# Kernel optimization log

Hardware: AMD Instinct MI355X
Metric: run time of the kernel (lower is better)

## Reference

```python
import jax, jax.numpy as jnp
import numpy as np

N_NODES = 1_000_000
N_UPD = 131_072
H = 128        # memory_dim
D_MSG = 256    # message_dim


def setup_inputs() -> dict:
    key = jax.random.key(0)
    ks = jax.random.split(key, 7)
    s_ih = 1.0 / np.sqrt(H)
    return {
        "memory": jax.random.normal(ks[0], (N_NODES, H), dtype=jnp.float32),
        "node_ids": jax.random.randint(ks[1], (N_UPD,), 0, N_NODES),
        "messages": jax.random.normal(ks[2], (N_UPD, D_MSG), dtype=jnp.float32),
        "W_ih": jax.random.uniform(ks[3], (3 * H, D_MSG), minval=-s_ih, maxval=s_ih, dtype=jnp.float32),
        "W_hh": jax.random.uniform(ks[4], (3 * H, H), minval=-s_ih, maxval=s_ih, dtype=jnp.float32),
        "b_ih": jax.random.uniform(ks[5], (3 * H,), minval=-s_ih, maxval=s_ih, dtype=jnp.float32),
        "b_hh": jax.random.uniform(ks[6], (3 * H,), minval=-s_ih, maxval=s_ih, dtype=jnp.float32),
    }


def _gru_cell(x, h, W_ih, W_hh, b_ih, b_hh):
    # torch GRUCell math. gates laid out as [r, z, n] along dim 0 of weights.
    gi = x @ W_ih.T + b_ih            # [M, 3H]
    gh = h @ W_hh.T + b_hh            # [M, 3H]
    i_r, i_z, i_n = jnp.split(gi, 3, axis=-1)
    h_r, h_z, h_n = jnp.split(gh, 3, axis=-1)
    r = jax.nn.sigmoid(i_r + h_r)
    z = jax.nn.sigmoid(i_z + h_z)
    n = jnp.tanh(i_n + r * h_n)
    return (1.0 - z) * n + z * h


def reference(memory, node_ids, messages, W_ih, W_hh, b_ih, b_hh):
    node_mem = memory[node_ids]                              # gather [M, H]
    updated = _gru_cell(messages, node_mem, W_ih, W_hh, b_ih, b_hh)
    return memory.at[node_ids].set(updated)                  # scatter back into full table
```

## Files before the change

### kernel.cpp

```cpp
#include <hip/hip_runtime.h>
#include <math.h>

#define NN     1000000
#define NUPD   131072
#define HDIM   128
#define DMSG   256
#define GRU_BLOCKS (NUPD / 64)
#define COPY_BLOCKS 4096

#define WI_OFF  0
#define WH_OFF  (384 * 256 * 2)
#define WIN_OFF (WH_OFF + 384 * 128 * 2)

typedef __attribute__((ext_vector_type(8))) short bf16x8;
typedef __attribute__((ext_vector_type(4))) float f32x4;

__device__ __forceinline__ short f2bf(float f) {
  unsigned u = __float_as_uint(f);
  unsigned r = (u + 0x7fffu + ((u >> 16) & 1u)) >> 16;
  return (short)r;
}
__device__ __forceinline__ float sigmoidf_fast(float x) {
  return 1.0f / (1.0f + __expf(-x));
}
__device__ __forceinline__ float tanhf_fast(float x) {
  return 1.0f - 2.0f / (__expf(2.0f * x) + 1.0f);
}

__global__ void mark_winner_kernel(const int* __restrict__ ids,
                                   int* __restrict__ w) {
  int j = blockIdx.x * blockDim.x + threadIdx.x;
  if (j < NUPD) atomicMax(&w[ids[j]], j);
}

__global__ void wconv_kernel(const float* __restrict__ Wi,
                             const float* __restrict__ Wh,
                             short* __restrict__ wi_bf,
                             short* __restrict__ wh_bf) {
  int i = blockIdx.x * blockDim.x + threadIdx.x;
  if (i < 384 * 256) {
    wi_bf[i] = f2bf(Wi[i]);
  } else {
    int j = i - 384 * 256;
    if (j < 384 * 128) wh_bf[j] = f2bf(Wh[j]);
  }
}

__launch_bounds__(512, 2)
__global__ void fat_kernel(const float* __restrict__ memory,
                           const int* __restrict__ node_ids,
                           const float* __restrict__ messages,
                           const short* __restrict__ Wi_bf,
                           const short* __restrict__ Wh_bf,
                           const float* __restrict__ b_ih,
                           const float* __restrict__ b_hh,
                           const int* __restrict__ winner,
                           float* __restrict__ out)
{
  __shared__ short xs[64][DMSG + 8];
  __shared__ short hs[64][HDIM + 8];
  __shared__ int   ids_s[64];
  __shared__ char  flag_s[64];

  const int tid = threadIdx.x;

  if (blockIdx.x >= GRU_BLOCKS) {
    const float4* __restrict__ src4 = (const float4*)memory;
    float4* __restrict__ dst4 = (float4*)out;
    const long long n4 = (long long)NN * (HDIM / 4);
    long long i = (long long)(blockIdx.x - GRU_BLOCKS) * 512 + tid;
    const long long stride = (long long)COPY_BLOCKS * 512;
    for (; i < n4; i += stride) {
      int row = (int)(i >> 5);
      if (winner[row] < 0) dst4[i] = src4[i];
    }
    return;
  }

  const int row0 = blockIdx.x * 64;
  const int lane = tid & 63;
  const int wv   = tid >> 6;

  if (tid < 64) {
    int id = node_ids[row0 + tid];
    ids_s[tid] = id;
    flag_s[tid] = (winner[id] == row0 + tid) ? 1 : 0;
  }

  {
    int r = tid >> 5;
    int c8 = tid & 31;
#pragma unroll
    for (int it = 0; it < 4; ++it) {
      const float4* p4 = (const float4*)(messages + (size_t)(row0 + r + it * 16) * DMSG);
      float4 v0 = p4[c8 * 2];
      float4 v1 = p4[c8 * 2 + 1];
      bf16x8 o;
      o[0] = f2bf(v0.x); o[1] = f2bf(v0.y); o[2] = f2bf(v0.z); o[3] = f2bf(v0.w);
      o[4] = f2bf(v1.x); o[5] = f2bf(v1.y); o[6] = f2bf(v1.z); o[7] = f2bf(v1.w);
      *(bf16x8*)&xs[r + it * 16][c8 * 8] = o;
    }
  }

  {
    int r = tid >> 3;
    int c16 = (tid & 7) * 16;
    int id = node_ids[row0 + r];
    const float4* p4 = (const float4*)(memory + (size_t)id * HDIM + c16);
    float4 v0 = p4[0], v1 = p4[1], v2 = p4[2], v3 = p4[3];
    bf16x8 o0, o1;
    o0[0] = f2bf(v0.x); o0[1] = f2bf(v0.y); o0[2] = f2bf(v0.z); o0[3] = f2bf(v0.w);
    o0[4] = f2bf(v1.x); o0[5] = f2bf(v1.y); o0[6] = f2bf(v1.z); o0[7] = f2bf(v1.w);
    o1[0] = f2bf(v2.x); o1[1] = f2bf(v2.y); o1[2] = f2bf(v2.z); o1[3] = f2bf(v2.w);
    o1[4] = f2bf(v3.x); o1[5] = f2bf(v3.y); o1[6] = f2bf(v3.z); o1[7] = f2bf(v3.w);
    *(bf16x8*)&hs[r][c16] = o0;
    *(bf16x8*)&hs[r][c16 + 8] = o1;
  }

  __syncthreads();

  const int g0  = __builtin_amdgcn_readfirstlane(wv * 16);
  const int col = lane & 15;
  const int kg  = lane >> 4;

  f32x4 acc_r[4]  = {{0,0,0,0},{0,0,0,0},{0,0,0,0},{0,0,0,0}};
  f32x4 acc_z[4]  = {{0,0,0,0},{0,0,0,0},{0,0,0,0},{0,0,0,0}};
  f32x4 acc_in[4] = {{0,0,0,0},{0,0,0,0},{0,0,0,0},{0,0,0,0}};
  f32x4 acc_hn[4] = {{0,0,0,0},{0,0,0,0},{0,0,0,0},{0,0,0,0}};

  {
    const short* wr = Wi_bf + (size_t)(g0 + col) * DMSG;
    const short* wz = Wi_bf + (size_t)(g0 + 128 + col) * DMSG;
    const short* wn = Wi_bf + (size_t)(g0 + 256 + col) * DMSG;
#pragma unroll
    for (int ks = 0; ks < 8; ++ks) {
      const int ko = ks * 32 + kg * 8;
      bf16x8 br = *(const bf16x8*)(wr + ko);
      bf16x8 bz = *(const bf16x8*)(wz + ko);
      bf16x8 bn = *(const bf16x8*)(wn + ko);
#pragma unroll
      for (int rt = 0; rt < 4; ++rt) {
        bf16x8 a = *(const bf16x8*)&xs[rt * 16 + col][ko];
        acc_r[rt]  = __builtin_amdgcn_mfma_f32_16x16x32_bf16(a, br, acc_r[rt], 0, 0, 0);
        acc_z[rt]  = __builtin_amdgcn_mfma_f32_16x16x32_bf16(a, bz, acc_z[rt], 0, 0, 0);
        acc_in[rt] = __builtin_amdgcn_mfma_f32_16x16x32_bf16(a, bn, acc_in[rt], 0, 0, 0);
      }
    }
  }

  {
    const short* wr = Wh_bf + (size_t)(g0 + col) * HDIM;
    const short* wz = Wh_bf + (size_t)(g0 + 128 + col) * HDIM;
    const short* wn = Wh_bf + (size_t)(g0 + 256 + col) * HDIM;
#pragma unroll
    for (int ks = 0; ks < 4; ++ks) {
      const int ko = ks * 32 + kg * 8;
      bf16x8 br = *(const bf16x8*)(wr + ko);
      bf16x8 bz = *(const bf16x8*)(wz + ko);
      bf16x8 bn = *(const bf16x8*)(wn + ko);
#pragma unroll
      for (int rt = 0; rt < 4; ++rt) {
        bf16x8 a = *(const bf16x8*)&hs[rt * 16 + col][ko];
        acc_r[rt]  = __builtin_amdgcn_mfma_f32_16x16x32_bf16(a, br, acc_r[rt], 0, 0, 0);
        acc_z[rt]  = __builtin_amdgcn_mfma_f32_16x16x32_bf16(a, bz, acc_z[rt], 0, 0, 0);
        acc_hn[rt] = __builtin_amdgcn_mfma_f32_16x16x32_bf16(a, bn, acc_hn[rt], 0, 0, 0);
      }
    }
  }

  const int g = g0 + col;
  const float bias_r  = b_ih[g] + b_hh[g];
  const float bias_z  = b_ih[g + 128] + b_hh[g + 128];
  const float bias_in = b_ih[g + 256];
  const float bias_hn = b_hh[g + 256];

#pragma unroll
  for (int rt = 0; rt < 4; ++rt) {
#pragma unroll
    for (int reg = 0; reg < 4; ++reg) {
      const int row = rt * 16 + kg * 4 + reg;
      const int id  = ids_s[row];
      float r = sigmoidf_fast(acc_r[rt][reg] + bias_r);
      float z = sigmoidf_fast(acc_z[rt][reg] + bias_z);
      float n = tanhf_fast(acc_in[rt][reg] + bias_in + r * (acc_hn[rt][reg] + bias_hn));
      float h = memory[(size_t)id * HDIM + g];
      float nh = (1.0f - z) * n + z * h;
      if (flag_s[row]) out[(size_t)id * HDIM + g] = nh;
    }
  }
}

extern "C" void kernel_launch(void* const* d_in, const int* in_sizes, int n_in,
                              void* d_out, int out_size, void* d_ws, size_t ws_size,
                              hipStream_t stream) {
  const float* memory   = (const float*)d_in[0];
  const int*   node_ids = (const int*)  d_in[1];
  const float* messages = (const float*)d_in[2];
  const float* W_ih     = (const float*)d_in[3];
  const float* W_hh     = (const float*)d_in[4];
  const float* b_ih     = (const float*)d_in[5];
  const float* b_hh     = (const float*)d_in[6];
  float* out = (float*)d_out;

  char* ws = (char*)d_ws;
  short* Wi_bf  = (short*)(ws + WI_OFF);
  short* Wh_bf  = (short*)(ws + WH_OFF);
  int*   winner = (int*)  (ws + WIN_OFF);

  hipMemsetAsync(winner, 0xFF, (size_t)NN * sizeof(int), stream);
  mark_winner_kernel<<<NUPD / 256, 256, 0, stream>>>(node_ids, winner);
  wconv_kernel<<<(384 * 256 + 384 * 128 + 255) / 256, 256, 0, stream>>>(
      W_ih, W_hh, Wi_bf, Wh_bf);

  fat_kernel<<<GRU_BLOCKS + COPY_BLOCKS, 512, 0, stream>>>(
      memory, node_ids, messages, Wi_bf, Wh_bf, b_ih, b_hh, winner, out);
}
```

Measured before the change: 355.5 us.

## Interleave copy and GRU blocks, shrink GRU tiles, batch winner loads, merge prep kernels

```diff
diff --git a/kernel.cpp b/kernel.cpp
--- a/kernel.cpp
+++ b/kernel.cpp
@@ -5,8 +5,14 @@
 #define NUPD   131072
 #define HDIM   128
 #define DMSG   256
-#define GRU_BLOCKS (NUPD / 64)
-#define COPY_BLOCKS 4096
+
+#define GRU_ROWS    16
+#define GRU_BLOCKS  (NUPD / GRU_ROWS)
+#define COPY_BLOCKS 8192
+#define TOTAL_BLOCKS (GRU_BLOCKS + COPY_BLOCKS)
+#define COPY_STRIDE  (COPY_BLOCKS * 256)
+#define COPY_ITERS   16
+#define N4_TOTAL     ((long long)NN * (HDIM / 4))
 
 #define WI_OFF  0
 #define WH_OFF  (384 * 256 * 2)
@@ -27,26 +33,20 @@
   return 1.0f - 2.0f / (__expf(2.0f * x) + 1.0f);
 }
 
-__global__ void mark_winner_kernel(const int* __restrict__ ids,
-                                   int* __restrict__ w) {
-  int j = blockIdx.x * blockDim.x + threadIdx.x;
-  if (j < NUPD) atomicMax(&w[ids[j]], j);
-}
-
-__global__ void wconv_kernel(const float* __restrict__ Wi,
-                             const float* __restrict__ Wh,
-                             short* __restrict__ wi_bf,
-                             short* __restrict__ wh_bf) {
-  int i = blockIdx.x * blockDim.x + threadIdx.x;
-  if (i < 384 * 256) {
-    wi_bf[i] = f2bf(Wi[i]);
-  } else {
-    int j = i - 384 * 256;
-    if (j < 384 * 128) wh_bf[j] = f2bf(Wh[j]);
-  }
-}
-
-__launch_bounds__(512, 2)
+__global__ void prep_kernel(const int* __restrict__ ids,
+                            const float* __restrict__ Wi,
+                            const float* __restrict__ Wh,
+                            short* __restrict__ wi_bf,
+                            short* __restrict__ wh_bf,
+                            int* __restrict__ winner) {
+  int i = blockIdx.x * 256 + threadIdx.x;
+  if (i < NUPD) atomicMax(&winner[ids[i]], i);
+  if (i < 384 * 256) wi_bf[i] = f2bf(Wi[i]);
+  int j = i - 384 * 256;
+  if (j >= 0 && j < 384 * 128) wh_bf[j] = f2bf(Wh[j]);
+}
+
+__launch_bounds__(256, 5)
 __global__ void fat_kernel(const float* __restrict__ memory,
                            const int* __restrict__ node_ids,
                            const float* __restrict__ messages,
@@ -57,132 +57,127 @@
                            const int* __restrict__ winner,
                            float* __restrict__ out)
 {
-  __shared__ short xs[64][DMSG + 8];
-  __shared__ short hs[64][HDIM + 8];
-  __shared__ int   ids_s[64];
-  __shared__ char  flag_s[64];
+  __shared__ short xs[GRU_ROWS][DMSG + 8];
+  __shared__ short hs[GRU_ROWS][HDIM + 8];
+  __shared__ int   ids_s[GRU_ROWS];
+  __shared__ char  flag_s[GRU_ROWS];
 
   const int tid = threadIdx.x;
 
-  if (blockIdx.x >= GRU_BLOCKS) {
+  if (blockIdx.x & 1) {
+    const int ci = blockIdx.x >> 1;
     const float4* __restrict__ src4 = (const float4*)memory;
     float4* __restrict__ dst4 = (float4*)out;
-    const long long n4 = (long long)NN * (HDIM / 4);
-    long long i = (long long)(blockIdx.x - GRU_BLOCKS) * 512 + tid;
-    const long long stride = (long long)COPY_BLOCKS * 512;
-    for (; i < n4; i += stride) {
-      int row = (int)(i >> 5);
-      if (winner[row] < 0) dst4[i] = src4[i];
+    const long long base = (long long)ci * 256 + tid;
+
+    int w[COPY_ITERS];
+#pragma unroll
+    for (int it = 0; it < COPY_ITERS; ++it) {
+      long long i = base + (long long)it * COPY_STRIDE;
+      w[it] = (i < N4_TOTAL) ? winner[(int)(i >> 5)] : 0;
+    }
+#pragma unroll
+    for (int it = 0; it < COPY_ITERS; ++it) {
+      long long i = base + (long long)it * COPY_STRIDE;
+      if (i < N4_TOTAL && w[it] < 0) dst4[i] = src4[i];
     }
     return;
   }
 
-  const int row0 = blockIdx.x * 64;
+  const int gi   = blockIdx.x >> 1;
+  const int row0 = gi * GRU_ROWS;
   const int lane = tid & 63;
   const int wv   = tid >> 6;
 
-  if (tid < 64) {
+  if (tid < GRU_ROWS) {
     int id = node_ids[row0 + tid];
     ids_s[tid] = id;
     flag_s[tid] = (winner[id] == row0 + tid) ? 1 : 0;
   }
 
   {
-    int r = tid >> 5;
-    int c8 = tid & 31;
-#pragma unroll
-    for (int it = 0; it < 4; ++it) {
-      const float4* p4 = (const float4*)(messages + (size_t)(row0 + r + it * 16) * DMSG);
-      float4 v0 = p4[c8 * 2];
-      float4 v1 = p4[c8 * 2 + 1];
-      bf16x8 o;
-      o[0] = f2bf(v0.x); o[1] = f2bf(v0.y); o[2] = f2bf(v0.z); o[3] = f2bf(v0.w);
-      o[4] = f2bf(v1.x); o[5] = f2bf(v1.y); o[6] = f2bf(v1.z); o[7] = f2bf(v1.w);
-      *(bf16x8*)&xs[r + it * 16][c8 * 8] = o;
-    }
-  }
-
-  {
-    int r = tid >> 3;
-    int c16 = (tid & 7) * 16;
-    int id = node_ids[row0 + r];
-    const float4* p4 = (const float4*)(memory + (size_t)id * HDIM + c16);
+    int r = tid >> 4;
+    int c16 = (tid & 15) * 16;
+    const float4* p4 = (const float4*)(messages + (size_t)(row0 + r) * DMSG + c16);
     float4 v0 = p4[0], v1 = p4[1], v2 = p4[2], v3 = p4[3];
     bf16x8 o0, o1;
     o0[0] = f2bf(v0.x); o0[1] = f2bf(v0.y); o0[2] = f2bf(v0.z); o0[3] = f2bf(v0.w);
     o0[4] = f2bf(v1.x); o0[5] = f2bf(v1.y); o0[6] = f2bf(v1.z); o0[7] = f2bf(v1.w);
     o1[0] = f2bf(v2.x); o1[1] = f2bf(v2.y); o1[2] = f2bf(v2.z); o1[3] = f2bf(v2.w);
     o1[4] = f2bf(v3.x); o1[5] = f2bf(v3.y); o1[6] = f2bf(v3.z); o1[7] = f2bf(v3.w);
-    *(bf16x8*)&hs[r][c16] = o0;
-    *(bf16x8*)&hs[r][c16 + 8] = o1;
+    *(bf16x8*)&xs[r][c16]     = o0;
+    *(bf16x8*)&xs[r][c16 + 8] = o1;
+  }
+
+  {
+    int r = tid >> 4;
+    int c8 = (tid & 15) * 8;
+    int id = node_ids[row0 + r];
+    const float4* p4 = (const float4*)(memory + (size_t)id * HDIM + c8);
+    float4 v0 = p4[0], v1 = p4[1];
+    bf16x8 o;
+    o[0] = f2bf(v0.x); o[1] = f2bf(v0.y); o[2] = f2bf(v0.z); o[3] = f2bf(v0.w);
+    o[4] = f2bf(v1.x); o[5] = f2bf(v1.y); o[6] = f2bf(v1.z); o[7] = f2bf(v1.w);
+    *(bf16x8*)&hs[r][c8] = o;
   }
 
   __syncthreads();
 
-  const int g0  = __builtin_amdgcn_readfirstlane(wv * 16);
+  const int c0  = __builtin_amdgcn_readfirstlane(wv * 32);
   const int col = lane & 15;
   const int kg  = lane >> 4;
 
-  f32x4 acc_r[4]  = {{0,0,0,0},{0,0,0,0},{0,0,0,0},{0,0,0,0}};
-  f32x4 acc_z[4]  = {{0,0,0,0},{0,0,0,0},{0,0,0,0},{0,0,0,0}};
-  f32x4 acc_in[4] = {{0,0,0,0},{0,0,0,0},{0,0,0,0},{0,0,0,0}};
-  f32x4 acc_hn[4] = {{0,0,0,0},{0,0,0,0},{0,0,0,0},{0,0,0,0}};
-
-  {
-    const short* wr = Wi_bf + (size_t)(g0 + col) * DMSG;
-    const short* wz = Wi_bf + (size_t)(g0 + 128 + col) * DMSG;
-    const short* wn = Wi_bf + (size_t)(g0 + 256 + col) * DMSG;
-#pragma unroll
-    for (int ks = 0; ks < 8; ++ks) {
-      const int ko = ks * 32 + kg * 8;
-      bf16x8 br = *(const bf16x8*)(wr + ko);
-      bf16x8 bz = *(const bf16x8*)(wz + ko);
-      bf16x8 bn = *(const bf16x8*)(wn + ko);
-#pragma unroll
-      for (int rt = 0; rt < 4; ++rt) {
-        bf16x8 a = *(const bf16x8*)&xs[rt * 16 + col][ko];
-        acc_r[rt]  = __builtin_amdgcn_mfma_f32_16x16x32_bf16(a, br, acc_r[rt], 0, 0, 0);
-        acc_z[rt]  = __builtin_amdgcn_mfma_f32_16x16x32_bf16(a, bz, acc_z[rt], 0, 0, 0);
-        acc_in[rt] = __builtin_amdgcn_mfma_f32_16x16x32_bf16(a, bn, acc_in[rt], 0, 0, 0);
-      }
-    }
-  }
-
-  {
-    const short* wr = Wh_bf + (size_t)(g0 + col) * HDIM;
-    const short* wz = Wh_bf + (size_t)(g0 + 128 + col) * HDIM;
-    const short* wn = Wh_bf + (size_t)(g0 + 256 + col) * HDIM;
-#pragma unroll
-    for (int ks = 0; ks < 4; ++ks) {
-      const int ko = ks * 32 + kg * 8;
-      bf16x8 br = *(const bf16x8*)(wr + ko);
-      bf16x8 bz = *(const bf16x8*)(wz + ko);
-      bf16x8 bn = *(const bf16x8*)(wn + ko);
-#pragma unroll
-      for (int rt = 0; rt < 4; ++rt) {
-        bf16x8 a = *(const bf16x8*)&hs[rt * 16 + col][ko];
-        acc_r[rt]  = __builtin_amdgcn_mfma_f32_16x16x32_bf16(a, br, acc_r[rt], 0, 0, 0);
-        acc_z[rt]  = __builtin_amdgcn_mfma_f32_16x16x32_bf16(a, bz, acc_z[rt], 0, 0, 0);
-        acc_hn[rt] = __builtin_amdgcn_mfma_f32_16x16x32_bf16(a, bn, acc_hn[rt], 0, 0, 0);
-      }
-    }
-  }
-
-  const int g = g0 + col;
-  const float bias_r  = b_ih[g] + b_hh[g];
-  const float bias_z  = b_ih[g + 128] + b_hh[g + 128];
-  const float bias_in = b_ih[g + 256];
-  const float bias_hn = b_hh[g + 256];
-
-#pragma unroll
-  for (int rt = 0; rt < 4; ++rt) {
+  f32x4 acc_r[2]  = {{0,0,0,0},{0,0,0,0}};
+  f32x4 acc_z[2]  = {{0,0,0,0},{0,0,0,0}};
+  f32x4 acc_in[2] = {{0,0,0,0},{0,0,0,0}};
+  f32x4 acc_hn[2] = {{0,0,0,0},{0,0,0,0}};
+
+#pragma unroll
+  for (int ks = 0; ks < 8; ++ks) {
+    const int ko = ks * 32 + kg * 8;
+    bf16x8 a = *(const bf16x8*)&xs[col][ko];
+#pragma unroll
+    for (int ct = 0; ct < 2; ++ct) {
+      const int g = c0 + ct * 16 + col;
+      bf16x8 br = *(const bf16x8*)(Wi_bf + (size_t)(g)       * DMSG + ko);
+      bf16x8 bz = *(const bf16x8*)(Wi_bf + (size_t)(g + 128) * DMSG + ko);
+      bf16x8 bn = *(const bf16x8*)(Wi_bf + (size_t)(g + 256) * DMSG + ko);
+      acc_r[ct]  = __builtin_amdgcn_mfma_f32_16x16x32_bf16(a, br, acc_r[ct], 0, 0, 0);
+      acc_z[ct]  = __builtin_amdgcn_mfma_f32_16x16x32_bf16(a, bz, acc_z[ct], 0, 0, 0);
+      acc_in[ct] = __builtin_amdgcn_mfma_f32_16x16x32_bf16(a, bn, acc_in[ct], 0, 0, 0);
+    }
+  }
+
+#pragma unroll
+  for (int ks = 0; ks < 4; ++ks) {
+    const int ko = ks * 32 + kg * 8;
+    bf16x8 a = *(const bf16x8*)&hs[col][ko];
+#pragma unroll
+    for (int ct = 0; ct < 2; ++ct) {
+      const int g = c0 + ct * 16 + col;
+      bf16x8 br = *(const bf16x8*)(Wh_bf + (size_t)(g)       * HDIM + ko);
+      bf16x8 bz = *(const bf16x8*)(Wh_bf + (size_t)(g + 128) * HDIM + ko);
+      bf16x8 bn = *(const bf16x8*)(Wh_bf + (size_t)(g + 256) * HDIM + ko);
+      acc_r[ct]  = __builtin_amdgcn_mfma_f32_16x16x32_bf16(a, br, acc_r[ct], 0, 0, 0);
+      acc_z[ct]  = __builtin_amdgcn_mfma_f32_16x16x32_bf16(a, bz, acc_z[ct], 0, 0, 0);
+      acc_hn[ct] = __builtin_amdgcn_mfma_f32_16x16x32_bf16(a, bn, acc_hn[ct], 0, 0, 0);
+    }
+  }
+
+#pragma unroll
+  for (int ct = 0; ct < 2; ++ct) {
+    const int g = c0 + ct * 16 + col;
+    const float bias_r  = b_ih[g]       + b_hh[g];
+    const float bias_z  = b_ih[g + 128] + b_hh[g + 128];
+    const float bias_in = b_ih[g + 256];
+    const float bias_hn = b_hh[g + 256];
 #pragma unroll
     for (int reg = 0; reg < 4; ++reg) {
-      const int row = rt * 16 + kg * 4 + reg;
+      const int row = kg * 4 + reg;
       const int id  = ids_s[row];
-      float r = sigmoidf_fast(acc_r[rt][reg] + bias_r);
-      float z = sigmoidf_fast(acc_z[rt][reg] + bias_z);
-      float n = tanhf_fast(acc_in[rt][reg] + bias_in + r * (acc_hn[rt][reg] + bias_hn));
+      float r = sigmoidf_fast(acc_r[ct][reg] + bias_r);
+      float z = sigmoidf_fast(acc_z[ct][reg] + bias_z);
+      float n = tanhf_fast(acc_in[ct][reg] + bias_in + r * (acc_hn[ct][reg] + bias_hn));
       float h = memory[(size_t)id * HDIM + g];
       float nh = (1.0f - z) * n + z * h;
       if (flag_s[row]) out[(size_t)id * HDIM + g] = nh;
@@ -208,10 +203,9 @@
   int*   winner = (int*)  (ws + WIN_OFF);
 
   hipMemsetAsync(winner, 0xFF, (size_t)NN * sizeof(int), stream);
-  mark_winner_kernel<<<NUPD / 256, 256, 0, stream>>>(node_ids, winner);
-  wconv_kernel<<<(384 * 256 + 384 * 128 + 255) / 256, 256, 0, stream>>>(
-      W_ih, W_hh, Wi_bf, Wh_bf);
-
-  fat_kernel<<<GRU_BLOCKS + COPY_BLOCKS, 512, 0, stream>>>(
+  prep_kernel<<<(384 * 256 + 384 * 128 + 255) / 256, 256, 0, stream>>>(
+      node_ids, W_ih, W_hh, Wi_bf, Wh_bf, winner);
+
+  fat_kernel<<<TOTAL_BLOCKS, 256, 0, stream>>>(
       memory, node_ids, messages, Wi_bf, Wh_bf, b_ih, b_hh, winner, out);
 }
```

Result: slower. 625.5 us (+76.0%).
